# Kernel optimization log

Measured on AMD Instinct MI355X. Metric: run time of the kernel, lower is better.

## Reference

```python
import jax, jax.numpy as jnp
import numpy as np

B, T, NE = 8, 4096, 1024
E, TOPK = 16, 2
LIN = NE + 32 + NE // 4 + NE // 4 + NE // 8 + NE // 8  # 1824
N_CITIES = 4


def setup_inputs() -> dict:
    key = jax.random.key(0)
    ks = jax.random.split(key, 11)
    s = 1.0 / np.sqrt(LIN)
    return {
        "mh_output": jax.random.normal(ks[0], (B, T, NE), jnp.float32),
        "delta_t_info": jax.random.normal(ks[1], (B, T, NE // 4), jnp.float32),
        "delta_dis_info": jax.random.normal(ks[2], (B, T, NE // 4), jnp.float32),
        "delta_rg_info": jax.random.normal(ks[3], (B, T, NE // 8), jnp.float32),
        "delta_entropy_info": jax.random.normal(ks[4], (B, T, NE // 8), jnp.float32),
        "city_embeddings": jax.random.normal(ks[5], (N_CITIES, 32), jnp.float32),
        "w_route": jax.random.uniform(ks[6], (LIN, E), jnp.float32, -s, s),
        "b_route": jax.random.uniform(ks[7], (E,), jnp.float32, -s, s),
        "w_noise": jax.random.uniform(ks[8], (LIN, E), jnp.float32, -s, s),
        "b_noise": jax.random.uniform(ks[9], (E,), jnp.float32, -s, s),
        "noise_eps": jax.random.normal(ks[10], (B, T, E), jnp.float32),
        "city_index": 0,
    }


def reference(mh_output, delta_t_info, delta_dis_info, delta_rg_info,
              delta_entropy_info, city_embeddings, w_route, b_route,
              w_noise, b_noise, noise_eps, city_index):
    b, t, _ = mh_output.shape
    city_embed = city_embeddings[city_index]  # [32]
    city_embeds = jnp.broadcast_to(city_embed[None, None, :], (b, t, 32))
    x = jnp.concatenate([mh_output, city_embeds, delta_t_info, delta_dis_info,
                         delta_rg_info, delta_entropy_info], axis=-1)  # [B,T,LIN]
    logits = jnp.einsum('btf,fe->bte', x, w_route) + b_route
    noise_logits = jnp.einsum('btf,fe->bte', x, w_noise) + b_noise
    noisy_logits = logits + noise_eps * jax.nn.softplus(noise_logits)  # training path
    gate1 = jax.nn.softmax(noisy_logits, axis=-1)
    top_k_logits, indices = jax.lax.top_k(noisy_logits, TOPK)  # [B,T,K]
    # scatter top-k values into a -inf tensor == mask non-topk entries to -inf
    mask = jnp.sum(jax.nn.one_hot(indices, noisy_logits.shape[-1], dtype=jnp.bool_), axis=-2) > 0
    sparse_logits = jnp.where(mask, noisy_logits, -jnp.inf)
    router_output = jax.nn.softmax(sparse_logits, axis=-1)
    return router_output, indices, gate1
```

## Files before the change

### kernel.cpp

```cpp
#include <hip/hip_runtime.h>
#include <math.h>


#define TOKS 128
#define NCHUNK 28
#define I_OFF 524288
#define G_OFF 589824
#define SA 68
#define SW 36
#define SS 36

__device__ __forceinline__ float softplus_f(float x) {
  return fmaxf(x, 0.0f) + log1pf(expf(-fabsf(x)));
}

__device__ __forceinline__ float get_comp(const float4& v, int kk) {
  return kk == 0 ? v.x : kk == 1 ? v.y : kk == 2 ? v.z : v.w;
}

__global__ __launch_bounds__(512, 2) void router_kernel(
    const float* __restrict__ mh, const float* __restrict__ dt,
    const float* __restrict__ dd, const float* __restrict__ rg,
    const float* __restrict__ de, const float* __restrict__ cemb_all,
    const float* __restrict__ w_route, const float* __restrict__ b_route,
    const float* __restrict__ w_noise, const float* __restrict__ b_noise,
    const float* __restrict__ eps, const int* __restrict__ city_index,
    float* __restrict__ out) {
  __shared__ float smem[22016];
  __shared__ float city_l[32];
  float* sA0 = smem;
  float* sA1 = smem + 8704;
  float* sW0 = smem + 17408;
  float* sW1 = smem + 19712;
  float* sS  = smem;

  const int tid = threadIdx.x;
  const int w   = tid >> 6;
  const int ln  = tid & 63;
  const int tg  = ln & 15;
  const int eg  = ln >> 4;
  const int blockTok = blockIdx.x * TOKS;

  if (tid < 32) {
    const int e = tid & 15;
    const float* wsrc = (tid < 16) ? w_route : w_noise;
    const float* bsrc = (tid < 16) ? b_route : b_noise;
    const float* ce = cemb_all + city_index[0] * 32;
    float s = bsrc[e];
#pragma unroll
    for (int j = 0; j < 32; ++j) s = fmaf(ce[j], wsrc[(1024 + j) * 16 + e], s);
    city_l[tid] = s;
  }

  float4 accL[8], accH[8];
#pragma unroll
  for (int j = 0; j < 8; ++j) {
    accL[j] = make_float4(0.f, 0.f, 0.f, 0.f);
    accH[j] = make_float4(0.f, 0.f, 0.f, 0.f);
  }

  const int arow = tid >> 4, acol = (tid & 15) * 4;
  const int wrow = tid >> 3, wcol = tid & 7;

  float4 AR0, AR1, AR2, AR3, WR;

  auto a_src = [&](int g, int row) -> const float* {
    const float* base; int stride;
    if (g < 16)      { base = mh + g * 64;        stride = 1024; }
    else if (g < 20) { base = dt + (g - 16) * 64; stride = 256; }
    else if (g < 24) { base = dd + (g - 20) * 64; stride = 256; }
    else if (g < 26) { base = rg + (g - 24) * 64; stride = 128; }
    else             { base = de + (g - 26) * 64; stride = 128; }
    return base + (size_t)(blockTok + row) * stride;
  };

  auto prefetch = [&](int g) {
    AR0 = *(const float4*)(a_src(g, arow +  0) + acol);
    AR1 = *(const float4*)(a_src(g, arow + 32) + acol);
    AR2 = *(const float4*)(a_src(g, arow + 64) + acol);
    AR3 = *(const float4*)(a_src(g, arow + 96) + acol);
    const int kb = g * 64 + ((g >= 16) ? 32 : 0);
    const float* ws = (wcol < 4)
        ? (w_route + (kb + wrow) * 16 + wcol * 4)
        : (w_noise + (kb + wrow) * 16 + (wcol - 4) * 4);
    WR = *(const float4*)ws;
  };

  auto stage = [&](float* A, float* W) {
    *(float4*)&A[(arow +  0) * SA + acol] = AR0;
    *(float4*)&A[(arow + 32) * SA + acol] = AR1;
    *(float4*)&A[(arow + 64) * SA + acol] = AR2;
    *(float4*)&A[(arow + 96) * SA + acol] = AR3;
    *(float4*)&W[wrow * SW + wcol * 4] = WR;
  };

  prefetch(0);
  stage(sA0, sW0);
  __syncthreads();

  for (int c = 0; c < NCHUNK; ++c) {
    const float* A = (c & 1) ? sA1 : sA0;
    const float* W = (c & 1) ? sW1 : sW0;

    if (c + 1 < NCHUNK) prefetch(c + 1);

    const int k0 = w * 8;
#pragma unroll
    for (int q = 0; q < 2; ++q) {
      const int koff = k0 + q * 4;
      float4 a[8];
#pragma unroll
      for (int j = 0; j < 8; ++j)
        a[j] = *(const float4*)&A[(tg + 16 * j) * SA + koff];
#pragma unroll
      for (int kk = 0; kk < 4; ++kk) {
        float4 wv0 = *(const float4*)&W[(koff + kk) * SW + eg * 8];
        float4 wv1 = *(const float4*)&W[(koff + kk) * SW + eg * 8 + 4];
#pragma unroll
        for (int j = 0; j < 8; ++j) {
          const float s = get_comp(a[j], kk);
          accL[j].x = fmaf(s, wv0.x, accL[j].x);
          accL[j].y = fmaf(s, wv0.y, accL[j].y);
          accL[j].z = fmaf(s, wv0.z, accL[j].z);
          accL[j].w = fmaf(s, wv0.w, accL[j].w);
          accH[j].x = fmaf(s, wv1.x, accH[j].x);
          accH[j].y = fmaf(s, wv1.y, accH[j].y);
          accH[j].z = fmaf(s, wv1.z, accH[j].z);
          accH[j].w = fmaf(s, wv1.w, accH[j].w);
        }
      }
    }

    if (c + 1 < NCHUNK) stage((c & 1) ? sA0 : sA1, (c & 1) ? sW0 : sW1);
    __syncthreads();
  }

  for (int r = 0; r < 8; ++r) {
    if (w == r) {
#pragma unroll
      for (int j = 0; j < 8; ++j) {
        float* p = &sS[(tg + 16 * j) * SS + eg * 8];
        if (r == 0) {
          *(float4*)(p)     = accL[j];
          *(float4*)(p + 4) = accH[j];
        } else {
          float4 x0 = *(float4*)(p), x1 = *(float4*)(p + 4);
          x0.x += accL[j].x; x0.y += accL[j].y; x0.z += accL[j].z; x0.w += accL[j].w;
          x1.x += accH[j].x; x1.y += accH[j].y; x1.z += accH[j].z; x1.w += accH[j].w;
          *(float4*)(p)     = x0;
          *(float4*)(p + 4) = x1;
        }
      }
    }
    __syncthreads();
  }

  if (tid < TOKS) {
    const int tokg = blockTok + tid;
    float l[32];
#pragma unroll
    for (int e4 = 0; e4 < 8; ++e4) {
      float4 s0 = *(const float4*)&sS[tid * SS + e4 * 4];
      l[e4 * 4 + 0] = s0.x + ((e4 * 4 + 0 < 32) ? 0.f : 0.f);
      l[e4 * 4 + 0] = s0.x; l[e4 * 4 + 1] = s0.y;
      l[e4 * 4 + 2] = s0.z; l[e4 * 4 + 3] = s0.w;
    }
#pragma unroll
    for (int e = 0; e < 32; ++e) l[e] += city_l[e];

    const float* ep = eps + (size_t)tokg * 16;
    float n[16];
#pragma unroll
    for (int e = 0; e < 16; ++e)
      n[e] = fmaf(ep[e], softplus_f(l[16 + e]), l[e]);

    float m1 = -INFINITY; int i1 = 0;
#pragma unroll
    for (int e = 0; e < 16; ++e)
      if (n[e] > m1) { m1 = n[e]; i1 = e; }
    float m2 = -INFINITY; int i2 = 0;
#pragma unroll
    for (int e = 0; e < 16; ++e)
      if (e != i1 && n[e] > m2) { m2 = n[e]; i2 = e; }

    float ex[16], Z = 0.f;
#pragma unroll
    for (int e = 0; e < 16; ++e) { ex[e] = expf(n[e] - m1); Z += ex[e]; }
    const float invZ  = 1.0f / Z;
    const float invZ2 = 1.0f / (1.0f + expf(m2 - m1));

    float r[16], g1[16];
#pragma unroll
    for (int e = 0; e < 16; ++e) {
      r[e]  = (e == i1 || e == i2) ? ex[e] * invZ2 : 0.0f;
      g1[e] = ex[e] * invZ;
    }

    float* ro = out + (size_t)tokg * 16;
#pragma unroll
    for (int e4 = 0; e4 < 4; ++e4)
      *(float4*)(ro + e4 * 4) = make_float4(r[e4*4], r[e4*4+1], r[e4*4+2], r[e4*4+3]);

    out[I_OFF + (size_t)tokg * 2 + 0] = (float)i1;
    out[I_OFF + (size_t)tokg * 2 + 1] = (float)i2;

    float* go = out + G_OFF + (size_t)tokg * 16;
#pragma unroll
    for (int e4 = 0; e4 < 4; ++e4)
      *(float4*)(go + e4 * 4) = make_float4(g1[e4*4], g1[e4*4+1], g1[e4*4+2], g1[e4*4+3]);
  }
}

extern "C" void kernel_launch(void* const* d_in, const int* in_sizes, int n_in,
                              void* d_out, int out_size, void* d_ws, size_t ws_size,
                              hipStream_t stream) {
  const float* mh = (const float*)d_in[0];
  const float* dt = (const float*)d_in[1];
  const float* dd = (const float*)d_in[2];
  const float* rg = (const float*)d_in[3];
  const float* de = (const float*)d_in[4];
  const float* ce = (const float*)d_in[5];
  const float* wr = (const float*)d_in[6];
  const float* br = (const float*)d_in[7];
  const float* wn = (const float*)d_in[8];
  const float* bn = (const float*)d_in[9];
  const float* ep = (const float*)d_in[10];
  const int*   ci = (const int*)d_in[11];
  float* out = (float*)d_out;

  router_kernel<<<256, 512, 0, stream>>>(mh, dt, dd, rg, de, ce, wr, br, wn, bn,
                                         ep, ci, out);
}
```

Before: 296.5 us.

## Double threads per block and split K across 16 waves with two-buffer reduction

Launches 1024 threads per block instead of 512, so each wave handles 4 K-columns per chunk instead of 8. Each thread now loads half as many A rows, and only the first 512 threads load weights. The per-wave partial sums are reduced into two shared buffers, one per half of the waves, which are added in the epilogue. This is meant to add more waves for latency hiding in a memory-bound streaming GEMV, at the cost of higher register pressure limits (launch_bounds 1024,4) and a heavier reduction.

```diff
diff --git a/kernel.cpp b/kernel.cpp
--- a/kernel.cpp
+++ b/kernel.cpp
@@ -14,11 +14,17 @@
   return fmaxf(x, 0.0f) + log1pf(expf(-fabsf(x)));
 }
 
-__device__ __forceinline__ float get_comp(const float4& v, int kk) {
-  return kk == 0 ? v.x : kk == 1 ? v.y : kk == 2 ? v.z : v.w;
-}
-
-__global__ __launch_bounds__(512, 2) void router_kernel(
+#define FMA8(s, wa, wb, j)                         \
+  accL[j].x = fmaf(s, wa.x, accL[j].x);            \
+  accL[j].y = fmaf(s, wa.y, accL[j].y);            \
+  accL[j].z = fmaf(s, wa.z, accL[j].z);            \
+  accL[j].w = fmaf(s, wa.w, accL[j].w);            \
+  accH[j].x = fmaf(s, wb.x, accH[j].x);            \
+  accH[j].y = fmaf(s, wb.y, accH[j].y);            \
+  accH[j].z = fmaf(s, wb.z, accH[j].z);            \
+  accH[j].w = fmaf(s, wb.w, accH[j].w);
+
+__global__ __launch_bounds__(1024, 4) void router_kernel(
     const float* __restrict__ mh, const float* __restrict__ dt,
     const float* __restrict__ dd, const float* __restrict__ rg,
     const float* __restrict__ de, const float* __restrict__ cemb_all,
@@ -32,7 +38,8 @@
   float* sA1 = smem + 8704;
   float* sW0 = smem + 17408;
   float* sW1 = smem + 19712;
-  float* sS  = smem;
+  float* sS0 = smem;
+  float* sS1 = smem + 4608;
 
   const int tid = threadIdx.x;
   const int w   = tid >> 6;
@@ -59,10 +66,12 @@
     accH[j] = make_float4(0.f, 0.f, 0.f, 0.f);
   }
 
-  const int arow = tid >> 4, acol = (tid & 15) * 4;
-  const int wrow = tid >> 3, wcol = tid & 7;
-
-  float4 AR0, AR1, AR2, AR3, WR;
+  const int arow = tid >> 4;
+  const int acol = (tid & 15) * 4;
+  const int wrow = tid >> 3;
+  const int wcol = tid & 7;
+
+  float4 AR0, AR1, WR;
 
   auto a_src = [&](int g, int row) -> const float* {
     const float* base; int stride;
@@ -76,59 +85,50 @@
 
   auto prefetch = [&](int g) {
     AR0 = *(const float4*)(a_src(g, arow +  0) + acol);
-    AR1 = *(const float4*)(a_src(g, arow + 32) + acol);
-    AR2 = *(const float4*)(a_src(g, arow + 64) + acol);
-    AR3 = *(const float4*)(a_src(g, arow + 96) + acol);
-    const int kb = g * 64 + ((g >= 16) ? 32 : 0);
-    const float* ws = (wcol < 4)
-        ? (w_route + (kb + wrow) * 16 + wcol * 4)
-        : (w_noise + (kb + wrow) * 16 + (wcol - 4) * 4);
-    WR = *(const float4*)ws;
+    AR1 = *(const float4*)(a_src(g, arow + 64) + acol);
+    if (tid < 512) {
+      const int kb = g * 64 + ((g >= 16) ? 32 : 0);
+      const float* ws = (wcol < 4)
+          ? (w_route + (kb + wrow) * 16 + wcol * 4)
+          : (w_noise + (kb + wrow) * 16 + (wcol - 4) * 4);
+      WR = *(const float4*)ws;
+    }
   };
 
   auto stage = [&](float* A, float* W) {
     *(float4*)&A[(arow +  0) * SA + acol] = AR0;
-    *(float4*)&A[(arow + 32) * SA + acol] = AR1;
-    *(float4*)&A[(arow + 64) * SA + acol] = AR2;
-    *(float4*)&A[(arow + 96) * SA + acol] = AR3;
-    *(float4*)&W[wrow * SW + wcol * 4] = WR;
+    *(float4*)&A[(arow + 64) * SA + acol] = AR1;
+    if (tid < 512) *(float4*)&W[wrow * SW + wcol * 4] = WR;
   };
 
   prefetch(0);
   stage(sA0, sW0);
   __syncthreads();
 
+  const int k0 = w * 4;
+
   for (int c = 0; c < NCHUNK; ++c) {
     const float* A = (c & 1) ? sA1 : sA0;
     const float* W = (c & 1) ? sW1 : sW0;
 
     if (c + 1 < NCHUNK) prefetch(c + 1);
 
-    const int k0 = w * 8;
-#pragma unroll
-    for (int q = 0; q < 2; ++q) {
-      const int koff = k0 + q * 4;
-      float4 a[8];
-#pragma unroll
-      for (int j = 0; j < 8; ++j)
-        a[j] = *(const float4*)&A[(tg + 16 * j) * SA + koff];
-#pragma unroll
-      for (int kk = 0; kk < 4; ++kk) {
-        float4 wv0 = *(const float4*)&W[(koff + kk) * SW + eg * 8];
-        float4 wv1 = *(const float4*)&W[(koff + kk) * SW + eg * 8 + 4];
-#pragma unroll
-        for (int j = 0; j < 8; ++j) {
-          const float s = get_comp(a[j], kk);
-          accL[j].x = fmaf(s, wv0.x, accL[j].x);
-          accL[j].y = fmaf(s, wv0.y, accL[j].y);
-          accL[j].z = fmaf(s, wv0.z, accL[j].z);
-          accL[j].w = fmaf(s, wv0.w, accL[j].w);
-          accH[j].x = fmaf(s, wv1.x, accH[j].x);
-          accH[j].y = fmaf(s, wv1.y, accH[j].y);
-          accH[j].z = fmaf(s, wv1.z, accH[j].z);
-          accH[j].w = fmaf(s, wv1.w, accH[j].w);
-        }
-      }
+    float4 wA0 = *(const float4*)&W[(k0 + 0) * SW + eg * 8];
+    float4 wB0 = *(const float4*)&W[(k0 + 0) * SW + eg * 8 + 4];
+    float4 wA1 = *(const float4*)&W[(k0 + 1) * SW + eg * 8];
+    float4 wB1 = *(const float4*)&W[(k0 + 1) * SW + eg * 8 + 4];
+    float4 wA2 = *(const float4*)&W[(k0 + 2) * SW + eg * 8];
+    float4 wB2 = *(const float4*)&W[(k0 + 2) * SW + eg * 8 + 4];
+    float4 wA3 = *(const float4*)&W[(k0 + 3) * SW + eg * 8];
+    float4 wB3 = *(const float4*)&W[(k0 + 3) * SW + eg * 8 + 4];
+
+#pragma unroll
+    for (int j = 0; j < 8; ++j) {
+      float4 a = *(const float4*)&A[(tg + 16 * j) * SA + k0];
+      FMA8(a.x, wA0, wB0, j);
+      FMA8(a.y, wA1, wB1, j);
+      FMA8(a.z, wA2, wB2, j);
+      FMA8(a.w, wA3, wB3, j);
     }
 
     if (c + 1 < NCHUNK) stage((c & 1) ? sA0 : sA1, (c & 1) ? sW0 : sW1);
@@ -136,10 +136,11 @@
   }
 
   for (int r = 0; r < 8; ++r) {
-    if (w == r) {
+    if ((w & 7) == r) {
+      float* S = (w < 8) ? sS0 : sS1;
 #pragma unroll
       for (int j = 0; j < 8; ++j) {
-        float* p = &sS[(tg + 16 * j) * SS + eg * 8];
+        float* p = &S[(tg + 16 * j) * SS + eg * 8];
         if (r == 0) {
           *(float4*)(p)     = accL[j];
           *(float4*)(p + 4) = accH[j];
@@ -160,10 +161,12 @@
     float l[32];
 #pragma unroll
     for (int e4 = 0; e4 < 8; ++e4) {
-      float4 s0 = *(const float4*)&sS[tid * SS + e4 * 4];
-      l[e4 * 4 + 0] = s0.x + ((e4 * 4 + 0 < 32) ? 0.f : 0.f);
-      l[e4 * 4 + 0] = s0.x; l[e4 * 4 + 1] = s0.y;
-      l[e4 * 4 + 2] = s0.z; l[e4 * 4 + 3] = s0.w;
+      float4 s0 = *(const float4*)&sS0[tid * SS + e4 * 4];
+      float4 s1 = *(const float4*)&sS1[tid * SS + e4 * 4];
+      l[e4 * 4 + 0] = s0.x + s1.x;
+      l[e4 * 4 + 1] = s0.y + s1.y;
+      l[e4 * 4 + 2] = s0.z + s1.z;
+      l[e4 * 4 + 3] = s0.w + s1.w;
     }
 #pragma unroll
     for (int e = 0; e < 32; ++e) l[e] += city_l[e];
@@ -228,6 +231,6 @@
   const int*   ci = (const int*)d_in[11];
   float* out = (float*)d_out;
 
-  router_kernel<<<256, 512, 0, stream>>>(mh, dt, dd, rg, de, ce, wr, br, wn, bn,
-                                         ep, ci, out);
+  router_kernel<<<256, 1024, 0, stream>>>(mh, dt, dd, rg, de, ce, wr, br, wn, bn,
+                                          ep, ci, out);
 }
```

After: 461.2 us. +55.5%, slower.

## Restructure router GEMM: per-token lanes, wave-uniform scalar weight loads, tree reduction

Applied to the files above, without the earlier changes.

Halves the tokens per block to 64 and doubles the grid to 512 blocks. Each lane now owns one token and accumulates all 32 expert logits, reading the weights straight from global memory at wave-uniform addresses so they can become scalar loads instead of staging W in LDS. The serial 8-step cross-wave reduction becomes a 3-level tree reduction through padded LDS. This cuts LDS footprint and W staging traffic, in exchange for more per-lane accumulators and scalar weight loads inside the inner loop.

```diff
diff --git a/kernel.cpp b/kernel.cpp
--- a/kernel.cpp
+++ b/kernel.cpp
@@ -2,20 +2,15 @@
 #include <math.h>
 
 
-#define TOKS 128
+#define TOKS 64
 #define NCHUNK 28
 #define I_OFF 524288
 #define G_OFF 589824
-#define SA 68
-#define SW 36
-#define SS 36
+#define SA 65
+#define SP 33
 
 __device__ __forceinline__ float softplus_f(float x) {
   return fmaxf(x, 0.0f) + log1pf(expf(-fabsf(x)));
-}
-
-__device__ __forceinline__ float get_comp(const float4& v, int kk) {
-  return kk == 0 ? v.x : kk == 1 ? v.y : kk == 2 ? v.z : v.w;
 }
 
 __global__ __launch_bounds__(512, 2) void router_kernel(
@@ -26,19 +21,16 @@
     const float* __restrict__ w_noise, const float* __restrict__ b_noise,
     const float* __restrict__ eps, const int* __restrict__ city_index,
     float* __restrict__ out) {
-  __shared__ float smem[22016];
+  __shared__ float smem[8448];
   __shared__ float city_l[32];
   float* sA0 = smem;
-  float* sA1 = smem + 8704;
-  float* sW0 = smem + 17408;
-  float* sW1 = smem + 19712;
-  float* sS  = smem;
+  float* sA1 = smem + 4160;
 
   const int tid = threadIdx.x;
+  const int ln  = tid & 63;
   const int w   = tid >> 6;
-  const int ln  = tid & 63;
-  const int tg  = ln & 15;
-  const int eg  = ln >> 4;
+  const int wu  = __builtin_amdgcn_readfirstlane(w);
+  const int k0  = wu * 8;
   const int blockTok = blockIdx.x * TOKS;
 
   if (tid < 32) {
@@ -52,121 +44,112 @@
     city_l[tid] = s;
   }
 
-  float4 accL[8], accH[8];
-#pragma unroll
-  for (int j = 0; j < 8; ++j) {
-    accL[j] = make_float4(0.f, 0.f, 0.f, 0.f);
-    accH[j] = make_float4(0.f, 0.f, 0.f, 0.f);
-  }
-
-  const int arow = tid >> 4, acol = (tid & 15) * 4;
-  const int wrow = tid >> 3, wcol = tid & 7;
-
-  float4 AR0, AR1, AR2, AR3, WR;
+  float accR[16], accN[16];
+#pragma unroll
+  for (int e = 0; e < 16; ++e) { accR[e] = 0.f; accN[e] = 0.f; }
+
+  const int arow = tid >> 4;
+  const int acol = (tid & 15) * 4;
+
+  float4 AR0, AR1;
 
   auto a_src = [&](int g, int row) -> const float* {
     const float* base; int stride;
     if (g < 16)      { base = mh + g * 64;        stride = 1024; }
     else if (g < 20) { base = dt + (g - 16) * 64; stride = 256; }
     else if (g < 24) { base = dd + (g - 20) * 64; stride = 256; }
-    else if (g < 26) { base = rg + (g - 24) * 64; stride = 128; }
-    else             { base = de + (g - 26) * 64; stride = 128; }
+    else             { base = (g < 26) ? rg + (g - 24) * 64
+                                       : de + (g - 26) * 64;
+                       stride = 128; }
     return base + (size_t)(blockTok + row) * stride;
   };
 
   auto prefetch = [&](int g) {
     AR0 = *(const float4*)(a_src(g, arow +  0) + acol);
     AR1 = *(const float4*)(a_src(g, arow + 32) + acol);
-    AR2 = *(const float4*)(a_src(g, arow + 64) + acol);
-    AR3 = *(const float4*)(a_src(g, arow + 96) + acol);
-    const int kb = g * 64 + ((g >= 16) ? 32 : 0);
-    const float* ws = (wcol < 4)
-        ? (w_route + (kb + wrow) * 16 + wcol * 4)
-        : (w_noise + (kb + wrow) * 16 + (wcol - 4) * 4);
-    WR = *(const float4*)ws;
-  };
-
-  auto stage = [&](float* A, float* W) {
+  };
+
+  auto stage = [&](float* A) {
     *(float4*)&A[(arow +  0) * SA + acol] = AR0;
     *(float4*)&A[(arow + 32) * SA + acol] = AR1;
-    *(float4*)&A[(arow + 64) * SA + acol] = AR2;
-    *(float4*)&A[(arow + 96) * SA + acol] = AR3;
-    *(float4*)&W[wrow * SW + wcol * 4] = WR;
   };
 
   prefetch(0);
-  stage(sA0, sW0);
+  stage(sA0);
   __syncthreads();
 
   for (int c = 0; c < NCHUNK; ++c) {
     const float* A = (c & 1) ? sA1 : sA0;
-    const float* W = (c & 1) ? sW1 : sW0;
 
     if (c + 1 < NCHUNK) prefetch(c + 1);
 
-    const int k0 = w * 8;
-#pragma unroll
-    for (int q = 0; q < 2; ++q) {
-      const int koff = k0 + q * 4;
-      float4 a[8];
-#pragma unroll
-      for (int j = 0; j < 8; ++j)
-        a[j] = *(const float4*)&A[(tg + 16 * j) * SA + koff];
-#pragma unroll
-      for (int kk = 0; kk < 4; ++kk) {
-        float4 wv0 = *(const float4*)&W[(koff + kk) * SW + eg * 8];
-        float4 wv1 = *(const float4*)&W[(koff + kk) * SW + eg * 8 + 4];
-#pragma unroll
-        for (int j = 0; j < 8; ++j) {
-          const float s = get_comp(a[j], kk);
-          accL[j].x = fmaf(s, wv0.x, accL[j].x);
-          accL[j].y = fmaf(s, wv0.y, accL[j].y);
-          accL[j].z = fmaf(s, wv0.z, accL[j].z);
-          accL[j].w = fmaf(s, wv0.w, accL[j].w);
-          accH[j].x = fmaf(s, wv1.x, accH[j].x);
-          accH[j].y = fmaf(s, wv1.y, accH[j].y);
-          accH[j].z = fmaf(s, wv1.z, accH[j].z);
-          accH[j].w = fmaf(s, wv1.w, accH[j].w);
-        }
+    const int kb = c * 64 + ((c >= 16) ? 32 : 0) + k0;
+    const float* wr = w_route + (size_t)kb * 16;
+    const float* wn = w_noise + (size_t)kb * 16;
+
+    float4 a0 = *(const float4*)&A[ln * SA + k0];
+    float4 a1 = *(const float4*)&A[ln * SA + k0 + 4];
+
+#pragma unroll
+    for (int r = 0; r < 8; ++r) {
+      const float ak = (r == 0) ? a0.x : (r == 1) ? a0.y : (r == 2) ? a0.z
+                     : (r == 3) ? a0.w : (r == 4) ? a1.x : (r == 5) ? a1.y
+                     : (r == 6) ? a1.z : a1.w;
+#pragma unroll
+      for (int e = 0; e < 16; ++e) {
+        accR[e] = fmaf(wr[r * 16 + e], ak, accR[e]);
+        accN[e] = fmaf(wn[r * 16 + e], ak, accN[e]);
       }
     }
 
-    if (c + 1 < NCHUNK) stage((c & 1) ? sA0 : sA1, (c & 1) ? sW0 : sW1);
+    if (c + 1 < NCHUNK) stage((c & 1) ? sA0 : sA1);
     __syncthreads();
   }
 
-  for (int r = 0; r < 8; ++r) {
-    if (w == r) {
-#pragma unroll
-      for (int j = 0; j < 8; ++j) {
-        float* p = &sS[(tg + 16 * j) * SS + eg * 8];
-        if (r == 0) {
-          *(float4*)(p)     = accL[j];
-          *(float4*)(p + 4) = accH[j];
-        } else {
-          float4 x0 = *(float4*)(p), x1 = *(float4*)(p + 4);
-          x0.x += accL[j].x; x0.y += accL[j].y; x0.z += accL[j].z; x0.w += accL[j].w;
-          x1.x += accH[j].x; x1.y += accH[j].y; x1.z += accH[j].z; x1.w += accH[j].w;
-          *(float4*)(p)     = x0;
-          *(float4*)(p + 4) = x1;
-        }
-      }
+  auto writeP = [&](int slot) {
+    float* p = &smem[slot * 2112 + ln * SP];
+    *(float4*)(p +  0) = make_float4(accR[0],  accR[1],  accR[2],  accR[3]);
+    *(float4*)(p +  4) = make_float4(accR[4],  accR[5],  accR[6],  accR[7]);
+    *(float4*)(p +  8) = make_float4(accR[8],  accR[9],  accR[10], accR[11]);
+    *(float4*)(p + 12) = make_float4(accR[12], accR[13], accR[14], accR[15]);
+    *(float4*)(p + 16) = make_float4(accN[0],  accN[1],  accN[2],  accN[3]);
+    *(float4*)(p + 20) = make_float4(accN[4],  accN[5],  accN[6],  accN[7]);
+    *(float4*)(p + 24) = make_float4(accN[8],  accN[9],  accN[10], accN[11]);
+    *(float4*)(p + 28) = make_float4(accN[12], accN[13], accN[14], accN[15]);
+  };
+  auto addP = [&](int slot) {
+    const float* p = &smem[slot * 2112 + ln * SP];
+    float4 x;
+    x = *(const float4*)(p +  0); accR[0] += x.x; accR[1] += x.y; accR[2] += x.z; accR[3] += x.w;
+    x = *(const float4*)(p +  4); accR[4] += x.x; accR[5] += x.y; accR[6] += x.z; accR[7] += x.w;
+    x = *(const float4*)(p +  8); accR[8] += x.x; accR[9] += x.y; accR[10] += x.z; accR[11] += x.w;
+    x = *(const float4*)(p + 12); accR[12] += x.x; accR[13] += x.y; accR[14] += x.z; accR[15] += x.w;
+    x = *(const float4*)(p + 16); accN[0] += x.x; accN[1] += x.y; accN[2] += x.z; accN[3] += x.w;
+    x = *(const float4*)(p + 20); accN[4] += x.x; accN[5] += x.y; accN[6] += x.z; accN[7] += x.w;
+    x = *(const float4*)(p + 24); accN[8] += x.x; accN[9] += x.y; accN[10] += x.z; accN[11] += x.w;
+    x = *(const float4*)(p + 28); accN[12] += x.x; accN[13] += x.y; accN[14] += x.z; accN[15] += x.w;
+  };
+
+  if (w >= 4) writeP(w - 4);
+  __syncthreads();
+  if (w < 4) addP(w);
+  __syncthreads();
+  if (w == 2 || w == 3) writeP(w - 2);
+  __syncthreads();
+  if (w < 2) addP(w);
+  __syncthreads();
+  if (w == 1) writeP(0);
+  __syncthreads();
+
+  if (w == 0) {
+    addP(0);
+    const int tokg = blockTok + ln;
+    float l[32];
+#pragma unroll
+    for (int e = 0; e < 16; ++e) {
+      l[e]      = accR[e] + city_l[e];
+      l[16 + e] = accN[e] + city_l[16 + e];
     }
-    __syncthreads();
-  }
-
-  if (tid < TOKS) {
-    const int tokg = blockTok + tid;
-    float l[32];
-#pragma unroll
-    for (int e4 = 0; e4 < 8; ++e4) {
-      float4 s0 = *(const float4*)&sS[tid * SS + e4 * 4];
-      l[e4 * 4 + 0] = s0.x + ((e4 * 4 + 0 < 32) ? 0.f : 0.f);
-      l[e4 * 4 + 0] = s0.x; l[e4 * 4 + 1] = s0.y;
-      l[e4 * 4 + 2] = s0.z; l[e4 * 4 + 3] = s0.w;
-    }
-#pragma unroll
-    for (int e = 0; e < 32; ++e) l[e] += city_l[e];
 
     const float* ep = eps + (size_t)tokg * 16;
     float n[16];
@@ -228,6 +211,6 @@
   const int*   ci = (const int*)d_in[11];
   float* out = (float*)d_out;
 
-  router_kernel<<<256, 512, 0, stream>>>(mh, dt, dd, rg, de, ce, wr, br, wn, bn,
+  router_kernel<<<512, 512, 0, stream>>>(mh, dt, dd, rg, de, ce, wr, br, wn, bn,
                                          ep, ci, out);
 }
```

Result: slower. 333.6 us (+12.5%).

## Use 1024-thread blocks, split tokens across two halves, read weights from global

Applied to the files above, without the earlier changes.

Doubles the block to 1024 threads. Two groups of 8 waves each take 64 of the block's 128 tokens, and each thread now accumulates 4 token rows instead of 8. Weight tiles are no longer staged in shared memory; each thread reads them straight from global memory (through the cache), which shrinks LDS use and drops the weight staging stores. The aim is more parallelism per block and less pressure on registers and LDS, at the cost of repeated global weight loads and heavier block-wide barriers.

```diff
diff --git a/kernel.cpp b/kernel.cpp
--- a/kernel.cpp
+++ b/kernel.cpp
@@ -7,18 +7,13 @@
 #define I_OFF 524288
 #define G_OFF 589824
 #define SA 68
-#define SW 36
-#define SS 36
+#define SP 36
 
 __device__ __forceinline__ float softplus_f(float x) {
   return fmaxf(x, 0.0f) + log1pf(expf(-fabsf(x)));
 }
 
-__device__ __forceinline__ float get_comp(const float4& v, int kk) {
-  return kk == 0 ? v.x : kk == 1 ? v.y : kk == 2 ? v.z : v.w;
-}
-
-__global__ __launch_bounds__(512, 2) void router_kernel(
+__global__ __launch_bounds__(1024, 1) void router_kernel(
     const float* __restrict__ mh, const float* __restrict__ dt,
     const float* __restrict__ dd, const float* __restrict__ rg,
     const float* __restrict__ de, const float* __restrict__ cemb_all,
@@ -26,17 +21,16 @@
     const float* __restrict__ w_noise, const float* __restrict__ b_noise,
     const float* __restrict__ eps, const int* __restrict__ city_index,
     float* __restrict__ out) {
-  __shared__ float smem[22016];
+  __shared__ float smem[17408];
   __shared__ float city_l[32];
   float* sA0 = smem;
   float* sA1 = smem + 8704;
-  float* sW0 = smem + 17408;
-  float* sW1 = smem + 19712;
-  float* sS  = smem;
 
   const int tid = threadIdx.x;
   const int w   = tid >> 6;
   const int ln  = tid & 63;
+  const int h   = w >> 3;
+  const int s   = w & 7;
   const int tg  = ln & 15;
   const int eg  = ln >> 4;
   const int blockTok = blockIdx.x * TOKS;
@@ -46,100 +40,100 @@
     const float* wsrc = (tid < 16) ? w_route : w_noise;
     const float* bsrc = (tid < 16) ? b_route : b_noise;
     const float* ce = cemb_all + city_index[0] * 32;
-    float s = bsrc[e];
-#pragma unroll
-    for (int j = 0; j < 32; ++j) s = fmaf(ce[j], wsrc[(1024 + j) * 16 + e], s);
-    city_l[tid] = s;
-  }
-
-  float4 accL[8], accH[8];
-#pragma unroll
-  for (int j = 0; j < 8; ++j) {
+    float sacc = bsrc[e];
+#pragma unroll
+    for (int j = 0; j < 32; ++j)
+      sacc = fmaf(ce[j], wsrc[(1024 + j) * 16 + e], sacc);
+    city_l[tid] = sacc;
+  }
+
+  float4 accL[4], accH[4];
+#pragma unroll
+  for (int j = 0; j < 4; ++j) {
     accL[j] = make_float4(0.f, 0.f, 0.f, 0.f);
     accH[j] = make_float4(0.f, 0.f, 0.f, 0.f);
   }
 
-  const int arow = tid >> 4, acol = (tid & 15) * 4;
-  const int wrow = tid >> 3, wcol = tid & 7;
-
-  float4 AR0, AR1, AR2, AR3, WR;
+  const int arow = tid >> 4;
+  const int acol = (tid & 15) * 4;
+
+  float4 AR0, AR1;
 
   auto a_src = [&](int g, int row) -> const float* {
     const float* base; int stride;
     if (g < 16)      { base = mh + g * 64;        stride = 1024; }
     else if (g < 20) { base = dt + (g - 16) * 64; stride = 256; }
     else if (g < 24) { base = dd + (g - 20) * 64; stride = 256; }
-    else if (g < 26) { base = rg + (g - 24) * 64; stride = 128; }
-    else             { base = de + (g - 26) * 64; stride = 128; }
+    else             { base = (g < 26) ? rg + (g - 24) * 64
+                                       : de + (g - 26) * 64;
+                       stride = 128; }
     return base + (size_t)(blockTok + row) * stride;
   };
 
   auto prefetch = [&](int g) {
     AR0 = *(const float4*)(a_src(g, arow +  0) + acol);
-    AR1 = *(const float4*)(a_src(g, arow + 32) + acol);
-    AR2 = *(const float4*)(a_src(g, arow + 64) + acol);
-    AR3 = *(const float4*)(a_src(g, arow + 96) + acol);
-    const int kb = g * 64 + ((g >= 16) ? 32 : 0);
-    const float* ws = (wcol < 4)
-        ? (w_route + (kb + wrow) * 16 + wcol * 4)
-        : (w_noise + (kb + wrow) * 16 + (wcol - 4) * 4);
-    WR = *(const float4*)ws;
+    AR1 = *(const float4*)(a_src(g, arow + 64) + acol);
   };
 
-  auto stage = [&](float* A, float* W) {
+  auto stage = [&](float* A) {
     *(float4*)&A[(arow +  0) * SA + acol] = AR0;
-    *(float4*)&A[(arow + 32) * SA + acol] = AR1;
-    *(float4*)&A[(arow + 64) * SA + acol] = AR2;
-    *(float4*)&A[(arow + 96) * SA + acol] = AR3;
-    *(float4*)&W[wrow * SW + wcol * 4] = WR;
+    *(float4*)&A[(arow + 64) * SA + acol] = AR1;
   };
 
   prefetch(0);
-  stage(sA0, sW0);
+  stage(sA0);
   __syncthreads();
+
+  const int abase = (h * 64 + tg) * SA + s * 8;
+  const float* wsel = (eg < 2) ? w_route : w_noise;
+  const int ec = (eg & 1) * 8;
 
   for (int c = 0; c < NCHUNK; ++c) {
     const float* A = (c & 1) ? sA1 : sA0;
-    const float* W = (c & 1) ? sW1 : sW0;
 
     if (c + 1 < NCHUNK) prefetch(c + 1);
 
-    const int k0 = w * 8;
-#pragma unroll
-    for (int q = 0; q < 2; ++q) {
-      const int koff = k0 + q * 4;
-      float4 a[8];
-#pragma unroll
-      for (int j = 0; j < 8; ++j)
-        a[j] = *(const float4*)&A[(tg + 16 * j) * SA + koff];
-#pragma unroll
-      for (int kk = 0; kk < 4; ++kk) {
-        float4 wv0 = *(const float4*)&W[(koff + kk) * SW + eg * 8];
-        float4 wv1 = *(const float4*)&W[(koff + kk) * SW + eg * 8 + 4];
-#pragma unroll
-        for (int j = 0; j < 8; ++j) {
-          const float s = get_comp(a[j], kk);
-          accL[j].x = fmaf(s, wv0.x, accL[j].x);
-          accL[j].y = fmaf(s, wv0.y, accL[j].y);
-          accL[j].z = fmaf(s, wv0.z, accL[j].z);
-          accL[j].w = fmaf(s, wv0.w, accL[j].w);
-          accH[j].x = fmaf(s, wv1.x, accH[j].x);
-          accH[j].y = fmaf(s, wv1.y, accH[j].y);
-          accH[j].z = fmaf(s, wv1.z, accH[j].z);
-          accH[j].w = fmaf(s, wv1.w, accH[j].w);
-        }
+    const int kb = c * 64 + ((c >= 16) ? 32 : 0);
+    const float* wb = wsel + (size_t)(kb + s * 8) * 16 + ec;
+
+    float4 aL[4], aH[4];
+#pragma unroll
+    for (int j = 0; j < 4; ++j) {
+      aL[j] = *(const float4*)&A[abase + j * (16 * SA)];
+      aH[j] = *(const float4*)&A[abase + j * (16 * SA) + 4];
+    }
+
+#pragma unroll
+    for (int k = 0; k < 8; ++k) {
+      const float4 w0 = *(const float4*)(wb + k * 16);
+      const float4 w1 = *(const float4*)(wb + k * 16 + 4);
+#pragma unroll
+      for (int j = 0; j < 4; ++j) {
+        const float ak =
+            (k == 0) ? aL[j].x : (k == 1) ? aL[j].y : (k == 2) ? aL[j].z
+          : (k == 3) ? aL[j].w : (k == 4) ? aH[j].x : (k == 5) ? aH[j].y
+          : (k == 6) ? aH[j].z : aH[j].w;
+        accL[j].x = fmaf(ak, w0.x, accL[j].x);
+        accL[j].y = fmaf(ak, w0.y, accL[j].y);
+        accL[j].z = fmaf(ak, w0.z, accL[j].z);
+        accL[j].w = fmaf(ak, w0.w, accL[j].w);
+        accH[j].x = fmaf(ak, w1.x, accH[j].x);
+        accH[j].y = fmaf(ak, w1.y, accH[j].y);
+        accH[j].z = fmaf(ak, w1.z, accH[j].z);
+        accH[j].w = fmaf(ak, w1.w, accH[j].w);
       }
     }
 
-    if (c + 1 < NCHUNK) stage((c & 1) ? sA0 : sA1, (c & 1) ? sW0 : sW1);
+    if (c + 1 < NCHUNK) stage((c & 1) ? sA0 : sA1);
     __syncthreads();
   }
 
   for (int r = 0; r < 8; ++r) {
-    if (w == r) {
-#pragma unroll
-      for (int j = 0; j < 8; ++j) {
-        float* p = &sS[(tg + 16 * j) * SS + eg * 8];
+    if (s == r) {
+      float* Sb = &smem[h * (64 * SP)];
+#pragma unroll
+      for (int j = 0; j < 4; ++j) {
+        float* p = &Sb[(tg + 16 * j) * SP + eg * 8];
         if (r == 0) {
           *(float4*)(p)     = accL[j];
           *(float4*)(p + 4) = accH[j];
@@ -157,11 +151,11 @@
 
   if (tid < TOKS) {
     const int tokg = blockTok + tid;
+    const float* Sb = &smem[(tid >> 6) * (64 * SP) + (tid & 63) * SP];
     float l[32];
 #pragma unroll
     for (int e4 = 0; e4 < 8; ++e4) {
-      float4 s0 = *(const float4*)&sS[tid * SS + e4 * 4];
-      l[e4 * 4 + 0] = s0.x + ((e4 * 4 + 0 < 32) ? 0.f : 0.f);
+      float4 s0 = *(const float4*)&Sb[e4 * 4];
       l[e4 * 4 + 0] = s0.x; l[e4 * 4 + 1] = s0.y;
       l[e4 * 4 + 2] = s0.z; l[e4 * 4 + 3] = s0.w;
     }
@@ -228,6 +222,6 @@
   const int*   ci = (const int*)d_in[11];
   float* out = (float*)d_out;
 
-  router_kernel<<<256, 512, 0, stream>>>(mh, dt, dd, rg, de, ce, wr, br, wn, bn,
-                                         ep, ci, out);
+  router_kernel<<<256, 1024, 0, stream>>>(mh, dt, dd, rg, de, ce, wr, br, wn, bn,
+                                          ep, ci, out);
 }
```

Result: slower. 333.8 us (+12.6%).
